# Optimization experiments

Hardware: AMD Instinct MI355X
Metric: run time of the kernel (lower is better)

The kernel has to match this reference:

```python
import jax, jax.numpy as jnp
import numpy as np

N_ROLES = 6
EPS = 1e-5

def _ln(x, scale, bias):
    m = jnp.mean(x, axis=-1, keepdims=True)
    v = jnp.var(x, axis=-1, keepdims=True)
    return (x - m) * jax.lax.rsqrt(v + EPS) * scale + bias

def setup_inputs() -> dict:
    key = jax.random.key(0)
    ks = jax.random.split(key, 20)
    T, B, D_OBS, H, A = 32, 1024, 256, 512, 32
    inp = {
        'rnn_states': jax.random.normal(ks[0], (B, H), jnp.float32),
        'obs': jax.random.normal(ks[1], (T, B, D_OBS), jnp.float32),
        'resets': jnp.zeros((T, B), jnp.float32),
        'available_actions': jnp.ones((T, B, A), jnp.float32),
        'role_ids': jax.random.randint(ks[2], (T, B), 0, N_ROLES, jnp.int32),
        # feature norm over obs_dim
        'fn_scale': jnp.ones((D_OBS,), jnp.float32),
        'fn_bias': jnp.zeros((D_OBS,), jnp.float32),
        # base MLP: obs_dim->512->512, each followed by LayerNorm
        'W0': jax.random.normal(ks[3], (D_OBS, H), jnp.float32) * 0.02,
        'b0': jnp.zeros((H,), jnp.float32),
        'ln0_scale': jnp.ones((H,), jnp.float32),
        'ln0_bias': jnp.zeros((H,), jnp.float32),
        'W1': jax.random.normal(ks[4], (H, H), jnp.float32) * 0.02,
        'b1': jnp.zeros((H,), jnp.float32),
        'ln1_scale': jnp.ones((H,), jnp.float32),
        'ln1_bias': jnp.zeros((H,), jnp.float32),
        # per-role routes: obs_dim->128->H (stacked over roles)
        'Wr0': jax.random.normal(ks[5], (N_ROLES, D_OBS, 128), jnp.float32) * 0.02,
        'br0': jnp.zeros((N_ROLES, 128), jnp.float32),
        'Wr1': jax.random.normal(ks[6], (N_ROLES, 128, H), jnp.float32) * 0.02,
        'br1': jnp.zeros((N_ROLES, H), jnp.float32),
        # per-role heads: H->64->32->action_dim (stacked over roles)
        'Wh0': jax.random.normal(ks[7], (N_ROLES, H, 64), jnp.float32) * 0.02,
        'bh0': jnp.zeros((N_ROLES, 64), jnp.float32),
        'Wh1': jax.random.normal(ks[8], (N_ROLES, 64, 32), jnp.float32) * 0.02,
        'bh1': jnp.zeros((N_ROLES, 32), jnp.float32),
        'Wh2': jax.random.normal(ks[9], (N_ROLES, 32, A), jnp.float32) * 0.02,
        'bh2': jnp.zeros((N_ROLES, A), jnp.float32),
    }
    return inp

def _gather_by_role(all_values, role_ids):
    # all_values: (K, T, B, F); role_ids: (T, B) -> (T, B, F)
    idx = role_ids[None, :, :, None].astype(jnp.int32)
    return jnp.take_along_axis(all_values, idx, axis=0)[0]

def reference(rnn_states, obs, resets, available_actions, role_ids,
              fn_scale, fn_bias, W0, b0, ln0_scale, ln0_bias,
              W1, b1, ln1_scale, ln1_bias,
              Wr0, br0, Wr1, br1,
              Wh0, bh0, Wh1, bh1, Wh2, bh2):
    # feature normalization on raw obs
    obs_n = _ln(obs, fn_scale, fn_bias)
    # shared base MLP (relu + LayerNorm after each Dense)
    e = _ln(jax.nn.relu(obs_n @ W0 + b0), ln0_scale, ln0_bias)
    e = _ln(jax.nn.relu(e @ W1 + b1), ln1_scale, ln1_bias)
    # per-role pre-GRU residual routes on (normalized) obs
    r = jax.nn.relu(jnp.einsum('tbi,kih->ktbh', obs_n, Wr0) + br0[:, None, None, :])
    r = jax.nn.relu(jnp.einsum('ktbh,kho->ktbo', r, Wr1) + br1[:, None, None, :])
    e = e + _gather_by_role(r, role_ids)
    # no recurrent policy configured: rnn_states pass through
    # per-role heads -> all logits (K, T, B, A)
    h = jax.nn.relu(jnp.einsum('tbh,khf->ktbf', e, Wh0) + bh0[:, None, None, :])
    h = jax.nn.relu(jnp.einsum('ktbf,kfg->ktbg', h, Wh1) + bh1[:, None, None, :])
    all_logits = jnp.einsum('ktbg,kga->ktba', h, Wh2) + bh2[:, None, None, :]
    logits = _gather_by_role(all_logits, role_ids)
    logits = jnp.where(available_actions > 0.5, logits, jnp.full_like(logits, -1e10))
    return rnn_states, logits
```

## Files before the change

kernel.cpp:

```cpp
#include <hip/hip_runtime.h>
#include <stdint.h>

typedef unsigned short u16;
typedef unsigned int u32;

using bf16x8 = __attribute__((ext_vector_type(8))) short;
using f32x4  = __attribute__((ext_vector_type(4))) float;

#define DEVINL __device__ __forceinline__

DEVINL float b2f(u16 u) { return __builtin_bit_cast(float, (u32)u << 16); }
DEVINL u16 f2b(float f) {
  u32 u = __builtin_bit_cast(u32, f);
  u += 0x7FFFu + ((u >> 16) & 1u);
  return (u16)(u >> 16);
}

DEVINL void gll16(const u16* src, u16* dst) {
  __builtin_amdgcn_global_load_lds(
      (const __attribute__((address_space(1))) void*)(uintptr_t)src,
      (__attribute__((address_space(3))) void*)(uintptr_t)dst, 16, 0, 0);
}

#define MFMA __builtin_amdgcn_mfma_f32_16x16x32_bf16
#define NROLE 6

DEVINL void tp_tile(const float* __restrict__ s, u16* __restrict__ d,
                    int R, int C, int bx, int by, int z)
{
  __shared__ u16 tile[32][33];
  const size_t mstride = (size_t)R * C;
  s += (size_t)z * mstride;
  d += (size_t)z * mstride;
  int r0 = bx * 32, c0 = by * 32;
  int tx = threadIdx.x & 31, ty = threadIdx.x >> 5;
#pragma unroll
  for (int i = 0; i < 32; i += 8)
    tile[ty + i][tx] = f2b(s[(size_t)(r0 + ty + i) * C + (c0 + tx)]);
  __syncthreads();
#pragma unroll
  for (int i = 0; i < 32; i += 8)
    d[(size_t)(c0 + ty + i) * R + (r0 + tx)] = tile[tx][ty + i];
}

__global__ __launch_bounds__(256) void mega0(
    const float* W0, const float* W1, const float* Wr0, const float* Wr1, const float* Wh0,
    u16* W0t, u16* W1t, u16* Wr0t, u16* Wr1t, u16* Wh0t,
    const float* __restrict__ obs, const float* __restrict__ fn_s,
    const float* __restrict__ fn_b, u16* __restrict__ obs_n,
    const int* __restrict__ rid, int* __restrict__ blkCnt,
    const float* __restrict__ rnn, float* __restrict__ outRnn)
{
  int b = blockIdx.x;
  const int tid = threadIdx.x;
  if (b < 1152) {
    if (b < 128)      {            tp_tile(W0, W0t, 256, 512, b % 8,  b / 8, 0); }
    else if (b < 384) { b -= 128;  tp_tile(W1, W1t, 512, 512, b % 16, b / 16, 0); }
    else if (b < 576) { b -= 384;  int t = b / 8;  tp_tile(Wr0, Wr0t, 256, 128, b % 8,  t % 4,  t / 4); }
    else if (b < 960) { b -= 576;  int t = b / 4;  tp_tile(Wr1, Wr1t, 128, 512, b % 4,  t % 16, t / 16); }
    else              { b -= 960;  int t = b / 16; tp_tile(Wh0, Wh0t, 512, 64,  b % 16, t % 2,  t / 2); }
  } else if (b < 3200) {
    b -= 1152;
    const int lane = tid & 63, wave = tid >> 6;
#pragma unroll
    for (int it = 0; it < 4; ++it) {
      int row = b * 16 + wave * 4 + it;
      const float* xr = obs + (size_t)row * 256 + lane * 4;
      float x[4] __attribute__((aligned(16)));
      *(float4*)x = *(const float4*)xr;
      float s = 0.f, s2 = 0.f;
#pragma unroll
      for (int p = 0; p < 4; ++p) { s += x[p]; s2 += x[p] * x[p]; }
#pragma unroll
      for (int o = 32; o > 0; o >>= 1) { s += __shfl_xor(s, o, 64); s2 += __shfl_xor(s2, o, 64); }
      float m = s * (1.f / 256.f);
      float v = s2 * (1.f / 256.f) - m * m;
      float inv = rsqrtf(v + 1e-5f);
      u16 yu[4] __attribute__((aligned(8)));
#pragma unroll
      for (int p = 0; p < 4; ++p)
        yu[p] = f2b((x[p] - m) * inv * fn_s[lane * 4 + p] + fn_b[lane * 4 + p]);
      *(uint2*)(obs_n + (size_t)row * 256 + lane * 4) = *(uint2*)yu;
    }
  } else if (b < 3328) {
    b -= 3200;
    __shared__ int h[NROLE];
    if (tid < NROLE) h[tid] = 0;
    __syncthreads();
    atomicAdd(&h[rid[b * 256 + tid]], 1);
    __syncthreads();
    if (tid < NROLE) blkCnt[b * NROLE + tid] = h[tid];
  } else {
    b -= 3328;
    const float4* src = (const float4*)rnn;
    float4* dst = (float4*)outRnn;
    int base = (b * 256 + tid) * 4;
#pragma unroll
    for (int i = 0; i < 4; ++i) dst[base + i] = src[base + i];
  }
}

__global__ __launch_bounds__(256) void fill2(
    const int* __restrict__ rid, const int* __restrict__ blkCnt,
    int* __restrict__ bucket, int* __restrict__ baseArr, int* __restrict__ cntArr)
{
  __shared__ int c[128 * NROLE];
  __shared__ int preArr[NROLE], scnt[NROLE], sbase[NROLE], h[NROLE];
  const int tid = threadIdx.x;
  const int bx = blockIdx.x;
  for (int i = tid; i < 128 * NROLE; i += 256) c[i] = blkCnt[i];
  if (tid < NROLE) h[tid] = 0;
  __syncthreads();
  if (tid < NROLE) {
    int k = tid, run = 0, pre = 0;
    for (int b = 0; b < 128; ++b) { if (b == bx) pre = run; run += c[b * NROLE + k]; }
    scnt[k] = run; preArr[k] = pre;
  }
  __syncthreads();
  if (tid == 0) {
    int r = 0;
    for (int k = 0; k < NROLE; ++k) { sbase[k] = r; r += scnt[k]; }
  }
  __syncthreads();
  if (bx == 0 && tid < NROLE) { baseArr[tid] = sbase[tid]; cntArr[tid] = scnt[tid]; }
  int i = bx * 256 + tid;
  int k = rid[i];
  int pos = atomicAdd(&h[k], 1);
  bucket[sbase[k] + preArr[k] + pos] = i;
}

template <int K>
__global__ __launch_bounds__(256, 2) void gemm_ln(
    const u16* __restrict__ A, const u16* __restrict__ Bt,
    const float* __restrict__ bias, const float* __restrict__ lnsc,
    const float* __restrict__ lnbi, u16* __restrict__ C)
{
  constexpr int BK = 128, NI = K / BK, NC = K / 32;
  __shared__ __align__(16) u16 As[2][64 * BK];
  __shared__ float redS[64][4];
  __shared__ float redSS[64][4];
  __shared__ float prm[1536];
  const int tid = threadIdx.x;
  const int rowBase = blockIdx.x * 64;
  const int lane = tid & 63, wave = tid >> 6;
#pragma unroll
  for (int i = tid; i < 512; i += 256) {
    prm[i] = bias[i]; prm[512 + i] = lnsc[i]; prm[1024 + i] = lnbi[i];
  }
  u32 aOff[4];
#pragma unroll
  for (int r = 0; r < 4; ++r) {
    int row = r * 16 + (tid >> 4);
    int chunk = tid & 15;
    aOff[r] = (u32)(rowBase + row) * (u32)K + (u32)((chunk ^ (row & 7)) * 8);
  }
  const int quad = lane >> 4, lm = lane & 15, l7 = lm & 7;
  const int wn = wave * 128;
  u32 bOff[8];
#pragma unroll
  for (int j = 0; j < 8; ++j)
    bOff[j] = (u32)(wn + j * 16 + lm) * (u32)K + (u32)(quad * 8);

  f32x4 acc[4][8] = {};

#pragma unroll
  for (int r = 0; r < 4; ++r)
    gll16(A + aOff[r], &As[0][r * 2048 + wave * 512]);
  bf16x8 bP[8];
#pragma unroll
  for (int j = 0; j < 8; ++j)
    bP[j] = *(const bf16x8*)(Bt + bOff[j]);
  __syncthreads();

  for (int i = 0; i < NI; ++i) {
    const u16* Ab = As[i & 1];
    if (i + 1 < NI) {
#pragma unroll
      for (int r = 0; r < 4; ++r)
        gll16(A + aOff[r] + (i + 1) * BK, &As[(i + 1) & 1][r * 2048 + wave * 512]);
    }
#pragma unroll
    for (int c = 0; c < 4; ++c) {
      const int g = i * 4 + c;
      bf16x8 bN[8];
      if (g + 1 < NC) {
#pragma unroll
        for (int j = 0; j < 8; ++j)
          bN[j] = *(const bf16x8*)(Bt + bOff[j] + (g + 1) * 32);
      }
      const int kc = c * 4;
      bf16x8 af[4];
#pragma unroll
      for (int i2 = 0; i2 < 4; ++i2)
        af[i2] = *(const bf16x8*)&Ab[(i2 * 16 + lm) * BK + (((quad + kc) ^ l7) * 8)];
#pragma unroll
      for (int i2 = 0; i2 < 4; ++i2)
#pragma unroll
        for (int j = 0; j < 8; ++j)
          acc[i2][j] = MFMA(af[i2], bP[j], acc[i2][j], 0, 0, 0);
      if (g + 1 < NC) {
#pragma unroll
        for (int j = 0; j < 8; ++j) bP[j] = bN[j];
      }
    }
    __syncthreads();
  }

#pragma unroll
  for (int i2 = 0; i2 < 4; ++i2) {
#pragma unroll
    for (int r2 = 0; r2 < 4; ++r2) {
      float s = 0.f, ss = 0.f;
#pragma unroll
      for (int j = 0; j < 8; ++j) {
        float v = fmaxf(acc[i2][j][r2] + prm[wn + j * 16 + lm], 0.f);
        acc[i2][j][r2] = v;
        s += v; ss += v * v;
      }
#pragma unroll
      for (int o = 1; o < 16; o <<= 1) { s += __shfl_xor(s, o, 64); ss += __shfl_xor(ss, o, 64); }
      if (lm == 0) {
        int rowL = i2 * 16 + quad * 4 + r2;
        redS[rowL][wave] = s;
        redSS[rowL][wave] = ss;
      }
    }
  }
  __syncthreads();
#pragma unroll
  for (int i2 = 0; i2 < 4; ++i2) {
#pragma unroll
    for (int r2 = 0; r2 < 4; ++r2) {
      int rowL = i2 * 16 + quad * 4 + r2;
      float ts  = redS[rowL][0] + redS[rowL][1] + redS[rowL][2] + redS[rowL][3];
      float tss = redSS[rowL][0] + redSS[rowL][1] + redSS[rowL][2] + redSS[rowL][3];
      float m = ts * (1.f / 512.f);
      float var = tss * (1.f / 512.f) - m * m;
      float inv = rsqrtf(var + 1e-5f);
      size_t base = (size_t)(rowBase + rowL) * 512;
#pragma unroll
      for (int j = 0; j < 8; ++j) {
        int col = wn + j * 16 + lm;
        float y = (acc[i2][j][r2] - m) * inv * prm[512 + col] + prm[1024 + col];
        C[base + col] = f2b(y);
      }
    }
  }
}

__global__ __launch_bounds__(256, 3) void route_head(
    const u16* __restrict__ obs_n, const u16* __restrict__ e,
    const u16* __restrict__ Wr0t, const float* __restrict__ br0,
    const u16* __restrict__ Wr1t, const float* __restrict__ br1,
    const u16* __restrict__ Wh0t, const float* __restrict__ bh0,
    const float* __restrict__ Wh1, const float* __restrict__ bh1,
    const float* __restrict__ Wh2, const float* __restrict__ bh2,
    const float* __restrict__ avail,
    const int* __restrict__ bucket, const int* __restrict__ baseArr,
    const int* __restrict__ cntArr, float* __restrict__ outLogits)
{
  __shared__ __align__(16) u16 sm[24960];
  __shared__ float prm[704];
  const int tid = threadIdx.x;

  int role = 0, rem = blockIdx.x, cnt;
  for (;;) {
    cnt = cntArr[role];
    int tiles = (cnt + 31) >> 5;
    if (rem < tiles) break;
    rem -= tiles;
    if (++role >= NROLE) return;
  }
  const int limit = cnt;
  const int rowBase = rem * 32;
  const int roleBase = baseArr[role];

  const int lane = tid & 63, wave = tid >> 6;
  const int quad = lane >> 4, lm = lane & 15, l7 = lm & 7;

#pragma unroll
  for (int r = 0; r < 4; ++r) {
    int lrow = r * 8 + (tid >> 5);
    int i = rowBase + lrow;
    if (i >= limit) i = rowBase;
    int grow = bucket[roleBase + i];
    gll16(obs_n + (u32)grow * 256u + (u32)(((tid & 31) ^ (lrow & 7)) * 8),
          &sm[16384 + r * 2048 + wave * 512]);
  }
#pragma unroll
  for (int r = 0; r < 8; ++r) {
    int lrow = r * 4 + wave;
    int i = rowBase + lrow;
    if (i >= limit) i = rowBase;
    int grow = bucket[roleBase + i];
    int chunk = tid & 63;
    int sw = (chunk & 56) | ((chunk ^ lrow) & 7);
    gll16(e + (u32)grow * 512u + (u32)(sw * 8), &sm[r * 2048 + wave * 512]);
  }
  {
    if (tid < 128) prm[tid] = br0[role * 128 + tid];
    for (int i = tid; i < 512; i += 256) prm[128 + i] = br1[role * 512 + i];
    if (tid < 64) prm[640 + tid] = bh0[role * 64 + tid];
  }
  __syncthreads();

  const int wn0 = wave * 32;
  const u16* B0 = Wr0t + (size_t)role * 128 * 256;
  f32x4 acc0[2][2] = {};
  bf16x8 b0R[2][2];
#pragma unroll
  for (int p = 0; p < 2; ++p)
#pragma unroll
    for (int j = 0; j < 2; ++j)
      b0R[p][j] = *(const bf16x8*)(B0 + (u32)(wn0 + j * 16 + lm) * 256u + (u32)(quad * 8 + p * 32));
#pragma unroll
  for (int it = 0; it < 8; ++it) {
    bf16x8 cur0 = b0R[it & 1][0], cur1 = b0R[it & 1][1];
    if (it + 2 < 8) {
#pragma unroll
      for (int j = 0; j < 2; ++j)
        b0R[it & 1][j] = *(const bf16x8*)(B0 + (u32)(wn0 + j * 16 + lm) * 256u + (u32)(quad * 8 + (it + 2) * 32));
    }
    const int kc = it * 4;
    bf16x8 af[2];
#pragma unroll
    for (int i2 = 0; i2 < 2; ++i2)
      af[i2] = *(const bf16x8*)&sm[16384 + (i2 * 16 + lm) * 256 + (((quad + kc) ^ l7) * 8)];
#pragma unroll
    for (int i2 = 0; i2 < 2; ++i2) {
      acc0[i2][0] = MFMA(af[i2], cur0, acc0[i2][0], 0, 0, 0);
      acc0[i2][1] = MFMA(af[i2], cur1, acc0[i2][1], 0, 0, 0);
    }
  }
  __syncthreads();
  u16* r1 = sm + 16384;
#pragma unroll
  for (int i2 = 0; i2 < 2; ++i2) {
#pragma unroll
    for (int r2 = 0; r2 < 4; ++r2) {
      int row = i2 * 16 + quad * 4 + r2;
#pragma unroll
      for (int j = 0; j < 2; ++j) {
        int col = wn0 + j * 16 + lm;
        float v = fmaxf(acc0[i2][j][r2] + prm[col], 0.f);
        r1[row * 128 + (((col >> 3) ^ (row & 7)) * 8) + (col & 7)] = f2b(v);
      }
    }
  }
  __syncthreads();

  const int wn1 = wave * 128;
  const u16* B1 = Wr1t + (size_t)role * 512 * 128;
  f32x4 acc1[2][8] = {};
  bf16x8 b1P[8];
#pragma unroll
  for (int j = 0; j < 8; ++j)
    b1P[j] = *(const bf16x8*)(B1 + (u32)(wn1 + j * 16 + lm) * 128u + (u32)(quad * 8));
#pragma unroll
  for (int kk = 0; kk < 128; kk += 32) {
    bf16x8 b1N[8];
    if (kk + 32 < 128) {
#pragma unroll
      for (int j = 0; j < 8; ++j)
        b1N[j] = *(const bf16x8*)(B1 + (u32)(wn1 + j * 16 + lm) * 128u + (u32)(quad * 8 + kk + 32));
    }
    const int kc = kk >> 3;
    bf16x8 af[2];
#pragma unroll
    for (int i2 = 0; i2 < 2; ++i2)
      af[i2] = *(const bf16x8*)&r1[(i2 * 16 + lm) * 128 + (((quad + kc) ^ l7) * 8)];
#pragma unroll
    for (int i2 = 0; i2 < 2; ++i2)
#pragma unroll
      for (int j = 0; j < 8; ++j)
        acc1[i2][j] = MFMA(af[i2], b1P[j], acc1[i2][j], 0, 0, 0);
    if (kk + 32 < 128) {
#pragma unroll
      for (int j = 0; j < 8; ++j) b1P[j] = b1N[j];
    }
  }
#pragma unroll
  for (int i2 = 0; i2 < 2; ++i2) {
#pragma unroll
    for (int r2 = 0; r2 < 4; ++r2) {
      int row = i2 * 16 + quad * 4 + r2;
#pragma unroll
      for (int j = 0; j < 8; ++j) {
        int col = wn1 + j * 16 + lm;
        int addr = row * 512 + (((col >> 3) ^ (row & 7)) * 8) + (col & 7);
        float v = fmaxf(acc1[i2][j][r2] + prm[128 + col], 0.f) + b2f(sm[addr]);
        sm[addr] = f2b(v);
      }
    }
  }
  __syncthreads();

  const int wn2 = wave * 16;
  const u16* B2 = Wh0t + (size_t)role * 64 * 512;
  f32x4 acc2[2] = {};
  bf16x8 b2R[4];
#pragma unroll
  for (int p = 0; p < 4; ++p)
    b2R[p] = *(const bf16x8*)(B2 + (u32)(wn2 + lm) * 512u + (u32)(quad * 8 + p * 32));
#pragma unroll
  for (int it = 0; it < 16; ++it) {
    bf16x8 cur = b2R[it & 3];
    if (it + 4 < 16)
      b2R[it & 3] = *(const bf16x8*)(B2 + (u32)(wn2 + lm) * 512u + (u32)(quad * 8 + (it + 4) * 32));
    const int kc = it * 4;
    bf16x8 af[2];
#pragma unroll
    for (int i2 = 0; i2 < 2; ++i2)
      af[i2] = *(const bf16x8*)&sm[(i2 * 16 + lm) * 512 + (((quad + kc) ^ l7) * 8)];
#pragma unroll
    for (int i2 = 0; i2 < 2; ++i2)
      acc2[i2] = MFMA(af[i2], cur, acc2[i2], 0, 0, 0);
  }
  u16* h0s = sm + 20480;
#pragma unroll
  for (int i2 = 0; i2 < 2; ++i2) {
#pragma unroll
    for (int r2 = 0; r2 < 4; ++r2) {
      int row = i2 * 16 + quad * 4 + r2;
      int col = wn2 + lm;
      h0s[row * 68 + col] = f2b(fmaxf(acc2[i2][r2] + prm[640 + col], 0.f));
    }
  }
  __syncthreads();

  {
    float* h1s = (float*)&sm[22656];
    const int r = tid >> 3;
    const int n0 = (tid & 7) * 4;
    const bool valid = (rowBase + r) < limit;
    const float* W1k = Wh1 + (size_t)role * 64 * 32;
    const float* W2k = Wh2 + (size_t)role * 32 * 32;
    float4 a1 = *(const float4*)(bh1 + role * 32 + n0);
#pragma unroll 8
    for (int j = 0; j < 64; ++j) {
      float hj = b2f(h0s[r * 68 + j]);
      float4 wv = *(const float4*)(W1k + j * 32 + n0);
      a1.x += hj * wv.x; a1.y += hj * wv.y; a1.z += hj * wv.z; a1.w += hj * wv.w;
    }
    h1s[r * 36 + n0 + 0] = fmaxf(a1.x, 0.f);
    h1s[r * 36 + n0 + 1] = fmaxf(a1.y, 0.f);
    h1s[r * 36 + n0 + 2] = fmaxf(a1.z, 0.f);
    h1s[r * 36 + n0 + 3] = fmaxf(a1.w, 0.f);
    __syncthreads();
    float4 a2 = *(const float4*)(bh2 + role * 32 + n0);
#pragma unroll 8
    for (int n = 0; n < 32; ++n) {
      float hn = h1s[r * 36 + n];
      float4 wv = *(const float4*)(W2k + n * 32 + n0);
      a2.x += hn * wv.x; a2.y += hn * wv.y; a2.z += hn * wv.z; a2.w += hn * wv.w;
    }
    if (valid) {
      int g = bucket[roleBase + rowBase + r];
      float4 av = *(const float4*)(avail + (size_t)g * 32 + n0);
      float4 o;
      o.x = (av.x > 0.5f) ? a2.x : -1e10f;
      o.y = (av.y > 0.5f) ? a2.y : -1e10f;
      o.z = (av.z > 0.5f) ? a2.z : -1e10f;
      o.w = (av.w > 0.5f) ? a2.w : -1e10f;
      *(float4*)(outLogits + (size_t)g * 32 + n0) = o;
    }
  }
}

extern "C" void kernel_launch(void* const* d_in, const int* in_sizes, int n_in,
                              void* d_out, int out_size, void* d_ws, size_t ws_size,
                              hipStream_t stream)
{
  const float* rnn  = (const float*)d_in[0];
  const float* obs  = (const float*)d_in[1];
  const float* avail= (const float*)d_in[3];
  const int*   rid  = (const int*)d_in[4];
  const float* fn_s = (const float*)d_in[5];
  const float* fn_b = (const float*)d_in[6];
  const float* W0   = (const float*)d_in[7];
  const float* b0   = (const float*)d_in[8];
  const float* ln0s = (const float*)d_in[9];
  const float* ln0b = (const float*)d_in[10];
  const float* W1   = (const float*)d_in[11];
  const float* b1   = (const float*)d_in[12];
  const float* ln1s = (const float*)d_in[13];
  const float* ln1b = (const float*)d_in[14];
  const float* Wr0  = (const float*)d_in[15];
  const float* br0  = (const float*)d_in[16];
  const float* Wr1  = (const float*)d_in[17];
  const float* br1  = (const float*)d_in[18];
  const float* Wh0  = (const float*)d_in[19];
  const float* bh0  = (const float*)d_in[20];
  const float* Wh1  = (const float*)d_in[21];
  const float* bh1  = (const float*)d_in[22];
  const float* Wh2  = (const float*)d_in[23];
  const float* bh2  = (const float*)d_in[24];

  const int ROWS = 32768;

  char* w = (char*)d_ws;
  auto carve = [&](size_t bytes) { char* p = w; w += (bytes + 255) & ~(size_t)255; return p; };
  u16* obs_n  = (u16*)carve((size_t)ROWS * 256 * 2);
  u16* bufA   = (u16*)carve((size_t)ROWS * 512 * 2);
  u16* bufB   = (u16*)carve((size_t)ROWS * 512 * 2);
  u16* W0t    = (u16*)carve((size_t)512 * 256 * 2);
  u16* W1t    = (u16*)carve((size_t)512 * 512 * 2);
  u16* Wr0t   = (u16*)carve((size_t)6 * 128 * 256 * 2);
  u16* Wr1t   = (u16*)carve((size_t)6 * 512 * 128 * 2);
  u16* Wh0t   = (u16*)carve((size_t)6 * 64 * 512 * 2);
  int* bucket = (int*)carve((size_t)ROWS * 4);
  int* blkCnt = (int*)carve((size_t)128 * NROLE * 4);
  int* baseArr= (int*)carve(256);
  int* cntArr = (int*)carve(256);

  float* outLogits = (float*)d_out + (size_t)1024 * 512;

  mega0<<<3456, 256, 0, stream>>>(W0, W1, Wr0, Wr1, Wh0, W0t, W1t, Wr0t, Wr1t, Wh0t,
                                  obs, fn_s, fn_b, obs_n, rid, blkCnt, rnn, (float*)d_out);

  fill2<<<128, 256, 0, stream>>>(rid, blkCnt, bucket, baseArr, cntArr);

  gemm_ln<256><<<512, 256, 0, stream>>>(obs_n, W0t, b0, ln0s, ln0b, bufA);
  gemm_ln<512><<<512, 256, 0, stream>>>(bufA, W1t, b1, ln1s, ln1b, bufB);

  route_head<<<1029, 256, 0, stream>>>(obs_n, bufB, Wr0t, br0, Wr1t, br1, Wh0t, bh0,
                                       Wh1, bh1, Wh2, bh2, avail,
                                       bucket, baseArr, cntArr, outLogits);
}
```

Baseline: 264.7 us.

## Shrink route_head LDS, load obs rows directly to registers, raise occupancy

The route_head kernel stops staging gathered obs rows in LDS. Each lane now loads its A fragments straight from global memory into registers, prefetched four steps ahead. Biases move from a shared param array into registers, the role lookup becomes an unrolled register scan, and h0/h1 scratch reuses the freed region, so LDS drops to 40KB and launch bounds rise to 4 blocks per CU. An extra barrier is added before the reused h1 buffer is written. In exchange, the uncoalesced per-lane global loads of A and the higher register pressure may offset the occupancy gain.

After: 290.1 us. +9.6%, slower.

```diff
diff --git a/kernel.cpp b/kernel.cpp
--- a/kernel.cpp
+++ b/kernel.cpp
@@ -248,7 +248,7 @@
   }
 }
 
-__global__ __launch_bounds__(256, 3) void route_head(
+__global__ __launch_bounds__(256, 4) void route_head(
     const u16* __restrict__ obs_n, const u16* __restrict__ e,
     const u16* __restrict__ Wr0t, const float* __restrict__ br0,
     const u16* __restrict__ Wr1t, const float* __restrict__ br1,
@@ -259,34 +259,33 @@
     const int* __restrict__ bucket, const int* __restrict__ baseArr,
     const int* __restrict__ cntArr, float* __restrict__ outLogits)
 {
-  __shared__ __align__(16) u16 sm[24960];
-  __shared__ float prm[704];
+  __shared__ __align__(16) u16 sm[20480];
   const int tid = threadIdx.x;
 
-  int role = 0, rem = blockIdx.x, cnt;
-  for (;;) {
-    cnt = cntArr[role];
-    int tiles = (cnt + 31) >> 5;
-    if (rem < tiles) break;
-    rem -= tiles;
-    if (++role >= NROLE) return;
-  }
+  int cA0, cA1, cA2, cA3, cA4, cA5, bA0, bA1, bA2, bA3, bA4, bA5;
+  {
+    int4 ca = *(const int4*)cntArr;  int2 cb = *(const int2*)(cntArr + 4);
+    int4 ba = *(const int4*)baseArr; int2 bb = *(const int2*)(baseArr + 4);
+    cA0 = ca.x; cA1 = ca.y; cA2 = ca.z; cA3 = ca.w; cA4 = cb.x; cA5 = cb.y;
+    bA0 = ba.x; bA1 = ba.y; bA2 = ba.z; bA3 = ba.w; bA4 = bb.x; bA5 = bb.y;
+  }
+  int role = -1, rem = blockIdx.x, cnt = 0, roleBase = 0;
+#define TRY_ROLE(k, ck, bk)                                        \
+  if (role < 0) {                                                  \
+    int tiles = ((ck) + 31) >> 5;                                  \
+    if (rem < tiles) { role = (k); cnt = (ck); roleBase = (bk); }  \
+    else rem -= tiles;                                             \
+  }
+  TRY_ROLE(0, cA0, bA0) TRY_ROLE(1, cA1, bA1) TRY_ROLE(2, cA2, bA2)
+  TRY_ROLE(3, cA3, bA3) TRY_ROLE(4, cA4, bA4) TRY_ROLE(5, cA5, bA5)
+#undef TRY_ROLE
+  if (role < 0) return;
   const int limit = cnt;
   const int rowBase = rem * 32;
-  const int roleBase = baseArr[role];
 
   const int lane = tid & 63, wave = tid >> 6;
   const int quad = lane >> 4, lm = lane & 15, l7 = lm & 7;
 
-#pragma unroll
-  for (int r = 0; r < 4; ++r) {
-    int lrow = r * 8 + (tid >> 5);
-    int i = rowBase + lrow;
-    if (i >= limit) i = rowBase;
-    int grow = bucket[roleBase + i];
-    gll16(obs_n + (u32)grow * 256u + (u32)(((tid & 31) ^ (lrow & 7)) * 8),
-          &sm[16384 + r * 2048 + wave * 512]);
-  }
 #pragma unroll
   for (int r = 0; r < 8; ++r) {
     int lrow = r * 4 + wave;
@@ -297,12 +296,16 @@
     int sw = (chunk & 56) | ((chunk ^ lrow) & 7);
     gll16(e + (u32)grow * 512u + (u32)(sw * 8), &sm[r * 2048 + wave * 512]);
   }
+
+  int growA0, growA1;
   {
-    if (tid < 128) prm[tid] = br0[role * 128 + tid];
-    for (int i = tid; i < 512; i += 256) prm[128 + i] = br1[role * 512 + i];
-    if (tid < 64) prm[640 + tid] = bh0[role * 64 + tid];
-  }
-  __syncthreads();
+    int i0 = rowBase + lm;        if (i0 >= limit) i0 = rowBase;
+    int i1 = rowBase + 16 + lm;   if (i1 >= limit) i1 = rowBase;
+    growA0 = bucket[roleBase + i0];
+    growA1 = bucket[roleBase + i1];
+  }
+  const u16* Ag0 = obs_n + (size_t)growA0 * 256;
+  const u16* Ag1 = obs_n + (size_t)growA1 * 256;
 
   const int wn0 = wave * 32;
   const u16* B0 = Wr0t + (size_t)role * 128 * 256;
@@ -313,26 +316,31 @@
 #pragma unroll
     for (int j = 0; j < 2; ++j)
       b0R[p][j] = *(const bf16x8*)(B0 + (u32)(wn0 + j * 16 + lm) * 256u + (u32)(quad * 8 + p * 32));
+  bf16x8 aR[4][2];
+#pragma unroll
+  for (int p = 0; p < 4; ++p) {
+    aR[p][0] = *(const bf16x8*)(Ag0 + (u32)(quad * 8 + p * 32));
+    aR[p][1] = *(const bf16x8*)(Ag1 + (u32)(quad * 8 + p * 32));
+  }
+  float bias0[2] = { br0[role * 128 + wn0 + lm], br0[role * 128 + wn0 + 16 + lm] };
 #pragma unroll
   for (int it = 0; it < 8; ++it) {
+    bf16x8 a0 = aR[it & 3][0], a1 = aR[it & 3][1];
     bf16x8 cur0 = b0R[it & 1][0], cur1 = b0R[it & 1][1];
     if (it + 2 < 8) {
 #pragma unroll
       for (int j = 0; j < 2; ++j)
         b0R[it & 1][j] = *(const bf16x8*)(B0 + (u32)(wn0 + j * 16 + lm) * 256u + (u32)(quad * 8 + (it + 2) * 32));
     }
-    const int kc = it * 4;
-    bf16x8 af[2];
-#pragma unroll
-    for (int i2 = 0; i2 < 2; ++i2)
-      af[i2] = *(const bf16x8*)&sm[16384 + (i2 * 16 + lm) * 256 + (((quad + kc) ^ l7) * 8)];
-#pragma unroll
-    for (int i2 = 0; i2 < 2; ++i2) {
-      acc0[i2][0] = MFMA(af[i2], cur0, acc0[i2][0], 0, 0, 0);
-      acc0[i2][1] = MFMA(af[i2], cur1, acc0[i2][1], 0, 0, 0);
-    }
-  }
-  __syncthreads();
+    if (it + 4 < 8) {
+      aR[it & 3][0] = *(const bf16x8*)(Ag0 + (u32)(quad * 8 + (it + 4) * 32));
+      aR[it & 3][1] = *(const bf16x8*)(Ag1 + (u32)(quad * 8 + (it + 4) * 32));
+    }
+    acc0[0][0] = MFMA(a0, cur0, acc0[0][0], 0, 0, 0);
+    acc0[0][1] = MFMA(a0, cur1, acc0[0][1], 0, 0, 0);
+    acc0[1][0] = MFMA(a1, cur0, acc0[1][0], 0, 0, 0);
+    acc0[1][1] = MFMA(a1, cur1, acc0[1][1], 0, 0, 0);
+  }
   u16* r1 = sm + 16384;
 #pragma unroll
   for (int i2 = 0; i2 < 2; ++i2) {
@@ -342,14 +350,17 @@
 #pragma unroll
       for (int j = 0; j < 2; ++j) {
         int col = wn0 + j * 16 + lm;
-        float v = fmaxf(acc0[i2][j][r2] + prm[col], 0.f);
+        float v = fmaxf(acc0[i2][j][r2] + bias0[j], 0.f);
         r1[row * 128 + (((col >> 3) ^ (row & 7)) * 8) + (col & 7)] = f2b(v);
       }
     }
   }
-  __syncthreads();
-
   const int wn1 = wave * 128;
+  float b1v[8];
+#pragma unroll
+  for (int j = 0; j < 8; ++j) b1v[j] = br1[role * 512 + wn1 + j * 16 + lm];
+  __syncthreads();
+
   const u16* B1 = Wr1t + (size_t)role * 512 * 128;
   f32x4 acc1[2][8] = {};
   bf16x8 b1P[8];
@@ -388,7 +399,7 @@
       for (int j = 0; j < 8; ++j) {
         int col = wn1 + j * 16 + lm;
         int addr = row * 512 + (((col >> 3) ^ (row & 7)) * 8) + (col & 7);
-        float v = fmaxf(acc1[i2][j][r2] + prm[128 + col], 0.f) + b2f(sm[addr]);
+        float v = fmaxf(acc1[i2][j][r2] + b1v[j], 0.f) + b2f(sm[addr]);
         sm[addr] = f2b(v);
       }
     }
@@ -397,6 +408,7 @@
 
   const int wn2 = wave * 16;
   const u16* B2 = Wh0t + (size_t)role * 64 * 512;
+  float b2v = bh0[role * 64 + wn2 + lm];
   f32x4 acc2[2] = {};
   bf16x8 b2R[4];
 #pragma unroll
@@ -416,20 +428,20 @@
     for (int i2 = 0; i2 < 2; ++i2)
       acc2[i2] = MFMA(af[i2], cur, acc2[i2], 0, 0, 0);
   }
-  u16* h0s = sm + 20480;
+  u16* h0s = sm + 16384;
 #pragma unroll
   for (int i2 = 0; i2 < 2; ++i2) {
 #pragma unroll
     for (int r2 = 0; r2 < 4; ++r2) {
       int row = i2 * 16 + quad * 4 + r2;
       int col = wn2 + lm;
-      h0s[row * 68 + col] = f2b(fmaxf(acc2[i2][r2] + prm[640 + col], 0.f));
+      h0s[row * 68 + col] = f2b(fmaxf(acc2[i2][r2] + b2v, 0.f));
     }
   }
   __syncthreads();
 
   {
-    float* h1s = (float*)&sm[22656];
+    float* h1s = (float*)&sm[16384];
     const int r = tid >> 3;
     const int n0 = (tid & 7) * 4;
     const bool valid = (rowBase + r) < limit;
@@ -442,10 +454,13 @@
       float4 wv = *(const float4*)(W1k + j * 32 + n0);
       a1.x += hj * wv.x; a1.y += hj * wv.y; a1.z += hj * wv.z; a1.w += hj * wv.w;
     }
-    h1s[r * 36 + n0 + 0] = fmaxf(a1.x, 0.f);
-    h1s[r * 36 + n0 + 1] = fmaxf(a1.y, 0.f);
-    h1s[r * 36 + n0 + 2] = fmaxf(a1.z, 0.f);
-    h1s[r * 36 + n0 + 3] = fmaxf(a1.w, 0.f);
+    a1.x = fmaxf(a1.x, 0.f); a1.y = fmaxf(a1.y, 0.f);
+    a1.z = fmaxf(a1.z, 0.f); a1.w = fmaxf(a1.w, 0.f);
+    __syncthreads();
+    h1s[r * 36 + n0 + 0] = a1.x;
+    h1s[r * 36 + n0 + 1] = a1.y;
+    h1s[r * 36 + n0 + 2] = a1.z;
+    h1s[r * 36 + n0 + 3] = a1.w;
     __syncthreads();
     float4 a2 = *(const float4*)(bh2 + role * 32 + n0);
 #pragma unroll 8
```
